# Performance work log

Hardware: AMD Instinct MI355X
Metric: run time of the kernel (lower is better)

Reference implementation:

```python
import jax, jax.numpy as jnp
import numpy as np

# ---- configuration (matches init_kwargs / input_specs) ----
N = 48        # velocity grid points per axis (unum = vnum = wnum)
B = 8         # spatial cells (batch)
QUAD = 8      # radial Gauss-Legendre quadrature points
OMEGA = 0.81  # VHS exponent used in the radial kernel weight r**omega
M_ANG = 5     # sphere-quadrature resolution -> M*(M-1) angle pairs
VMAX = 5.0    # velocity domain [-VMAX, VMAX]^3


def _besselj1(x):
    # Numerical Recipes rational approximation of J1(x), numpy, setup-time only.
    x = np.asarray(x, dtype=np.float64)
    ax = np.abs(x)
    y = x * x
    p1 = x * (72362614232.0 + y * (-7895059235.0 + y * (242396853.1
         + y * (-2972611.439 + y * (15704.48260 + y * (-30.16036606))))))
    q1 = 144725228442.0 + y * (2300535178.0 + y * (18583304.74
         + y * (99447.43394 + y * (376.9991397 + y))))
    small = p1 / q1
    axs = np.where(ax > 0, ax, 1.0)
    z = 8.0 / axs
    y2 = z * z
    p2 = 1.0 + y2 * (0.183105e-2 + y2 * (-0.3516396496e-4
         + y2 * (0.2457520174e-5 + y2 * (-0.240337019e-6))))
    q2 = 0.04687499995 + y2 * (-0.2002690873e-3 + y2 * (0.8449199096e-5
         + y2 * (-0.88228987e-6 + y2 * 0.105787412e-6)))
    xx = axs - 2.356194491  # ax - 3*pi/4
    big = np.sqrt(0.636619772 / axs) * (np.cos(xx) * p2 - z * np.sin(xx) * q2) * np.sign(x)
    return np.where(ax < 8.0, small, big)


def _init_kernel_mode_vector(n, quad_num, omega, m, vmax):
    # Fast spectral method precompute (Mouhot-Pareschi), mirrors init_kernel_mode_vector.
    pi = np.pi
    du = 2.0 * vmax / (n - 1)
    fre = np.arange(-(n // 2), n // 2).astype(np.float64) * (2.0 * pi / (n * du))
    supp = np.sqrt(2.0) * 2.0 * vmax / (3.0 + np.sqrt(2.0))
    xg, wg = np.polynomial.legendre.leggauss(quad_num)  # on [-1,1]
    r = 0.5 * supp * (xg + 1.0)   # radial abscissa on [0, supp]
    gw = 0.5 * supp * wg          # radial weights
    ta = pi / m * np.arange(1, m)      # (m-1,) polar angles
    tb = pi / m * np.arange(1, m + 1)  # (m,)  azimuthal angles
    st = np.sin(ta)[:, None, None, None, None]
    ct = np.cos(ta)[:, None, None, None, None]
    cb = np.cos(tb)[None, :, None, None, None]
    sb = np.sin(tb)[None, :, None, None, None]
    fx = fre[:, None, None]
    fy = fre[None, :, None]
    fz = fre[None, None, :]
    # s[a,b,i,j,k] = <freq, sigma(theta_a, theta2_b)>
    s = st * cb * fx + st * sb * fy + (ct * np.ones_like(sb)) * fz
    phi = np.zeros_like(s)
    for q in range(quad_num):  # small fixed quadrature loop (setup only)
        phi += 2.0 * gw[q] * (r[q] ** omega) * np.cos(s * r[q])
    phi *= st
    s2 = (fx ** 2 + fy ** 2 + fz ** 2) - s ** 2
    pos = s2 > 1e-12
    sr = np.sqrt(np.where(pos, s2, 1.0))
    psi = np.where(pos, 2.0 * pi * supp * _besselj1(supp * sr) / sr, pi * supp ** 2)
    phipsi = (phi * psi).sum(axis=(0, 1))
    t = (m - 1) * m
    return (phi.reshape(t, n, n, n).astype(np.float32),
            psi.reshape(t, n, n, n).astype(np.float32),
            phipsi.astype(np.float32))


def setup_inputs() -> dict:
    key = jax.random.key(0)
    k1, _ = jax.random.split(key)
    phi, psi, phipsi = _init_kernel_mode_vector(N, QUAD, OMEGA, M_ANG, VMAX)
    f = jax.random.uniform(k1, (B, N * N * N), dtype=jnp.float32)
    return {
        "f": f,
        "kn_bzm": jnp.ones((), dtype=jnp.float32),
        "phi": jnp.asarray(phi),
        "psi": jnp.asarray(psi),
        "phipsi": jnp.asarray(phipsi),
        "M": M_ANG,
    }


def reference(f, kn_bzm, phi, psi, phipsi, M):
    # do_collision: reshape flat velocity dim to 3D grid, run collision_fft.
    n = phi.shape[-1]
    axes = (-3, -2, -1)
    f3 = f.reshape(f.shape[:-1] + (n, n, n))
    nvel = n * n * n
    # normalized, shifted spectrum of f
    f_spec = jnp.fft.fftshift(
        jnp.fft.fftn(f3.astype(jnp.complex64), axes=axes) / nvel, axes=axes)
    # gain term: sum over M*(M-1) angle pairs of fft(f_spec*phi_t) * fft(f_spec*psi_t)
    fs = f_spec[..., None, :, :, :]                       # [B, 1, n, n, n]
    fg = (jnp.fft.fftn(fs * phi, axes=axes) *
          jnp.fft.fftn(fs * psi, axes=axes)).sum(axis=-4)  # [B, n, n, n]
    # loss term
    fl = (jnp.fft.fftn(f_spec * phipsi, axes=axes) *
          jnp.fft.fftn(f_spec, axes=axes))
    scale = (4.0 * jnp.pi ** 2) / kn_bzm / (M * M)
    Q = scale * (fg - fl).real
    return Q.reshape(f.shape).astype(f.dtype)
```

## Files before the change

kernel.cpp:

```cpp
#include <hip/hip_runtime.h>
#include <math.h>

#define NN 48
#define NP 49
#define N2 2304
#define N3 110592
#define NB 8
#define NT 20
#define NH 25
#define NSL 7

typedef float2 cplx;

#define CMAC(AR, AI, D, Wv)                                        \
    AR = fmaf((D).x, (Wv).x, AR); AR = fmaf(-(D).y, (Wv).y, AR);   \
    AI = fmaf((D).x, (Wv).y, AI); AI = fmaf((D).y, (Wv).x, AI);

#define CMAC4(AC, D, Wv)                                             \
    (AC).x = fmaf((D).x, (Wv).x, (AC).x); (AC).x = fmaf(-(D).y, (Wv).y, (AC).x); \
    (AC).y = fmaf((D).x, (Wv).y, (AC).y); (AC).y = fmaf((D).y, (Wv).x, (AC).y); \
    (AC).z = fmaf((D).z, (Wv).x, (AC).z); (AC).z = fmaf(-(D).w, (Wv).y, (AC).z); \
    (AC).w = fmaf((D).z, (Wv).y, (AC).w); (AC).w = fmaf((D).w, (Wv).x, (AC).w);

__device__ __forceinline__ void twinit(cplx* W, int t) {
    if (t < NN) {
        float ang = -6.28318530717958647692f * (float)t / (float)NN;
        float s, c;
        sincosf(ang, &s, &c);
        W[t] = make_float2(c, s);
    }
}

__device__ __forceinline__ void radix3_combine(
    float s0r, float s0i, float s1r, float s1i, float s2r, float s2i,
    cplx w1, cplx w2, cplx& X0, cplx& X1, cplx& X2)
{
    float y1r = s1r*w1.x - s1i*w1.y, y1i = s1r*w1.y + s1i*w1.x;
    float y2r = s2r*w2.x - s2i*w2.y, y2i = s2r*w2.y + s2i*w2.x;
    float ar = y1r + y2r, ai = y1i + y2i;
    float br = y1r - y2r, bi = y1i - y2i;
    X0 = make_float2(s0r + ar, s0i + ai);
    float mr = s0r - 0.5f*ar, mi = s0i - 0.5f*ai;
    const float h = 0.86602540378443864676f;
    X1 = make_float2(mr + h*bi, mi - h*br);
    X2 = make_float2(mr - h*bi, mi + h*br);
}

__device__ __forceinline__ void radix3_combine4(
    float4 s0, float4 s1, float4 s2, cplx w1, cplx w2,
    float4& X0, float4& X1, float4& X2)
{
    cplx a0, a1, a2, b0, b1, b2;
    radix3_combine(s0.x, s0.y, s1.x, s1.y, s2.x, s2.y, w1, w2, a0, a1, a2);
    radix3_combine(s0.z, s0.w, s1.z, s1.w, s2.z, s2.w, w1, w2, b0, b1, b2);
    X0 = make_float4(a0.x, a0.y, b0.x, b0.y);
    X1 = make_float4(a1.x, a1.y, b1.x, b1.y);
    X2 = make_float4(a2.x, a2.y, b2.x, b2.y);
}

__device__ __forceinline__ void dft_rows(cplx (*S)[NP], const cplx* W, int t, int shift) {
    const int rg = t >> 4;
    const int j  = t & 15;
    float ar[3][3], ai[3][3];
#pragma unroll
    for (int q = 0; q < 3; ++q)
#pragma unroll
        for (int r = 0; r < 3; ++r) { ar[q][r] = 0.f; ai[q][r] = 0.f; }
    const int step = 3 * j;
    int tw = 0;
#pragma unroll 4
    for (int n1 = 0; n1 < 16; ++n1) {
        cplx w = W[tw];
#pragma unroll
        for (int q = 0; q < 3; ++q) {
            const cplx* row = S[3*rg + q];
            cplx d0 = row[3*n1+0], d1 = row[3*n1+1], d2 = row[3*n1+2];
            CMAC(ar[q][0], ai[q][0], d0, w);
            CMAC(ar[q][1], ai[q][1], d1, w);
            CMAC(ar[q][2], ai[q][2], d2, w);
        }
        tw += step; if (tw >= NN) tw -= NN;
    }
    cplx w1 = W[j], w2 = W[2*j];
    __syncthreads();
    int k0 = j, k1 = j + 16, k2 = j + 32;
    if (shift) { k0 = (k0+24)%NN; k1 = (k1+24)%NN; k2 = (k2+24)%NN; }
#pragma unroll
    for (int q = 0; q < 3; ++q) {
        cplx X0, X1, X2;
        radix3_combine(ar[q][0],ai[q][0],ar[q][1],ai[q][1],ar[q][2],ai[q][2],w1,w2,X0,X1,X2);
        S[3*rg+q][k0] = X0; S[3*rg+q][k1] = X1; S[3*rg+q][k2] = X2;
    }
    __syncthreads();
}

__device__ __forceinline__ void dft_cols(cplx (*S)[NP], const cplx* W, int t, int shift) {
    const int zg = t & 15;
    const int j  = t >> 4;
    float ar[3][3], ai[3][3];
#pragma unroll
    for (int zi = 0; zi < 3; ++zi)
#pragma unroll
        for (int r = 0; r < 3; ++r) { ar[zi][r] = 0.f; ai[zi][r] = 0.f; }
    const int step = 3 * j;
    int tw = 0;
#pragma unroll 4
    for (int n1 = 0; n1 < 16; ++n1) {
        cplx w = W[tw];
#pragma unroll
        for (int r = 0; r < 3; ++r) {
            const cplx* row = S[3*n1 + r];
            cplx d0 = row[3*zg+0], d1 = row[3*zg+1], d2 = row[3*zg+2];
            CMAC(ar[0][r], ai[0][r], d0, w);
            CMAC(ar[1][r], ai[1][r], d1, w);
            CMAC(ar[2][r], ai[2][r], d2, w);
        }
        tw += step; if (tw >= NN) tw -= NN;
    }
    cplx w1 = W[j], w2 = W[2*j];
    __syncthreads();
    int k0 = j, k1 = j + 16, k2 = j + 32;
    if (shift) { k0 = (k0+24)%NN; k1 = (k1+24)%NN; k2 = (k2+24)%NN; }
#pragma unroll
    for (int zi = 0; zi < 3; ++zi) {
        cplx X0, X1, X2;
        radix3_combine(ar[zi][0],ai[zi][0],ar[zi][1],ai[zi][1],ar[zi][2],ai[zi][2],w1,w2,X0,X1,X2);
        S[k0][3*zg+zi] = X0; S[k1][3*zg+zi] = X1; S[k2][3*zg+zi] = X2;
    }
    __syncthreads();
}

__device__ __forceinline__ void dft_rows4(float4 (*S)[NP], const cplx* W, int t) {
    const int rg = t >> 4;
    const int j  = t & 15;
    float4 acc[3][3];
#pragma unroll
    for (int q = 0; q < 3; ++q)
#pragma unroll
        for (int r = 0; r < 3; ++r) acc[q][r] = make_float4(0.f,0.f,0.f,0.f);
    const int step = 3 * j;
    int tw = 0;
    const float4* r0 = S[3*rg + 0];
    const float4* r1 = S[3*rg + 1];
    const float4* r2 = S[3*rg + 2];
#pragma unroll 4
    for (int n1 = 0; n1 < 16; ++n1) {
        cplx w = W[tw];
        float4 d00 = r0[3*n1+0], d01 = r0[3*n1+1], d02 = r0[3*n1+2];
        float4 d10 = r1[3*n1+0], d11 = r1[3*n1+1], d12 = r1[3*n1+2];
        float4 d20 = r2[3*n1+0], d21 = r2[3*n1+1], d22 = r2[3*n1+2];
        CMAC4(acc[0][0], d00, w); CMAC4(acc[0][1], d01, w); CMAC4(acc[0][2], d02, w);
        CMAC4(acc[1][0], d10, w); CMAC4(acc[1][1], d11, w); CMAC4(acc[1][2], d12, w);
        CMAC4(acc[2][0], d20, w); CMAC4(acc[2][1], d21, w); CMAC4(acc[2][2], d22, w);
        tw += step; if (tw >= NN) tw -= NN;
    }
    cplx w1 = W[j], w2 = W[2*j];
    __syncthreads();
#pragma unroll
    for (int q = 0; q < 3; ++q) {
        float4 X0, X1, X2;
        radix3_combine4(acc[q][0], acc[q][1], acc[q][2], w1, w2, X0, X1, X2);
        S[3*rg+q][j] = X0; S[3*rg+q][j+16] = X1; S[3*rg+q][j+32] = X2;
    }
    __syncthreads();
}

__device__ __forceinline__ void dft_cols4(float4 (*S)[NP], const cplx* W, int t) {
    const int zg = t & 15;
    const int j  = t >> 4;
    float4 acc[3][3];
#pragma unroll
    for (int zi = 0; zi < 3; ++zi)
#pragma unroll
        for (int r = 0; r < 3; ++r) acc[zi][r] = make_float4(0.f,0.f,0.f,0.f);
    const int step = 3 * j;
    int tw = 0;
#pragma unroll 4
    for (int n1 = 0; n1 < 16; ++n1) {
        cplx w = W[tw];
#pragma unroll
        for (int r = 0; r < 3; ++r) {
            const float4* row = S[3*n1 + r];
            float4 d0 = row[3*zg+0], d1 = row[3*zg+1], d2 = row[3*zg+2];
            CMAC4(acc[0][r], d0, w);
            CMAC4(acc[1][r], d1, w);
            CMAC4(acc[2][r], d2, w);
        }
        tw += step; if (tw >= NN) tw -= NN;
    }
    cplx w1 = W[j], w2 = W[2*j];
    __syncthreads();
#pragma unroll
    for (int zi = 0; zi < 3; ++zi) {
        float4 X0, X1, X2;
        radix3_combine4(acc[zi][0], acc[zi][1], acc[zi][2], w1, w2, X0, X1, X2);
        S[j][3*zg+zi] = X0; S[j+16][3*zg+zi] = X1; S[j+32][3*zg+zi] = X2;
    }
    __syncthreads();
}

__global__ __launch_bounds__(256)
void kA_f(const float* __restrict__ f, cplx* __restrict__ out) {
    __shared__ cplx S[NN][NP];
    __shared__ cplx W[NN];
    const int x = blockIdx.x, b = blockIdx.y, t = threadIdx.x;
    const float* src = f + (size_t)b * N3 + (size_t)x * N2;
    for (int i = t; i < N2; i += 256) S[i / NN][i % NN] = make_float2(src[i], 0.f);
    twinit(W, t);
    __syncthreads();
    dft_rows(S, W, t, 1);
    dft_cols(S, W, t, 1);
    cplx* dst = out + (size_t)b * N3 + (size_t)x * N2;
    for (int i = t; i < N2; i += 256) dst[i] = S[i / NN][i % NN];
}

__global__ __launch_bounds__(256)
void kB_f(cplx* __restrict__ vol) {
    __shared__ cplx S[NN][NP];
    __shared__ cplx W[NN];
    const int y = blockIdx.x, b = blockIdx.y, t = threadIdx.x;
    cplx* base = vol + (size_t)b * N3 + (size_t)y * NN;
    for (int i = t; i < N2; i += 256) { int xr = i / NN, z = i % NN; S[xr][z] = base[(size_t)xr * N2 + z]; }
    twinit(W, t);
    __syncthreads();
    dft_cols(S, W, t, 1);
    const float inv = 1.f / (float)N3;
    for (int i = t; i < N2; i += 256) {
        int xr = i / NN, z = i % NN;
        cplx v = S[xr][z];
        base[(size_t)xr * N2 + z] = make_float2(v.x * inv, v.y * inv);
    }
}

__global__ __launch_bounds__(256)
void kAB(const cplx* __restrict__ spec,
         const float* __restrict__ phi, const float* __restrict__ psi,
         const float* __restrict__ phipsi,
         float4* __restrict__ vab, int t0) {
    __shared__ float4 S[NN][NP];
    __shared__ cplx W[NN];
    const int ix = blockIdx.x, b = blockIdx.y, lt = blockIdx.z, t = threadIdx.x;
    const int ti = t0 + lt;
    const cplx* src = spec + (size_t)b * N3 + (size_t)ix * N2;
    const float* mp;
    const float* mq;
    if (ti < NT) { mp = phi + (size_t)ti * N3 + (size_t)ix * N2; mq = psi + (size_t)ti * N3 + (size_t)ix * N2; }
    else         { mp = phipsi + (size_t)ix * N2;               mq = (const float*)nullptr; }
    for (int i = t; i < N2; i += 256) {
        cplx v = src[i];
        float p = mp[i];
        float q = mq ? mq[i] : 1.f;
        S[i / NN][i % NN] = make_float4(v.x * p, v.y * p, v.x * q, v.y * q);
    }
    twinit(W, t);
    __syncthreads();
    dft_rows4(S, W, t);
    dft_cols4(S, W, t);
    float4* out = vab + ((size_t)(lt * NB + b) * NH + ix) * N2;
    for (int i = t; i < N2; i += 256) out[i] = S[i / NN][i % NN];
}

__global__ __launch_bounds__(256)
void kB_all(const float4* __restrict__ vab,
            float* __restrict__ out, const float* __restrict__ kn,
            const int* __restrict__ Mv, int t0, int cn) {
    __shared__ float4 SAB[NH][NP];
    __shared__ cplx W[NN];
    const int y = blockIdx.x, b = blockIdx.y, s = blockIdx.z, t = threadIdx.x;
    twinit(W, t);
    const int zg = t & 15, jg = t >> 4;
    float qr[3][3];
#pragma unroll
    for (int m = 0; m < 3; ++m)
#pragma unroll
        for (int zi = 0; zi < 3; ++zi) qr[m][zi] = 0.f;

    for (int lt = s; lt < cn; lt += NSL) {
        const int ti = t0 + lt;
        const float4* pa = vab + (size_t)(lt * NB + b) * NH * N2 + (size_t)y * NN;
        for (int i = t; i < NH * NN; i += 256) {
            int n = i / NN, z = i % NN;
            SAB[n][z] = pa[(size_t)n * N2 + z];
        }
        __syncthreads();
        float sa[3][3], sb[3][3];
#pragma unroll
        for (int m = 0; m < 3; ++m)
#pragma unroll
            for (int zi = 0; zi < 3; ++zi) { sa[m][zi] = 0.f; sb[m][zi] = 0.f; }
        int m0 = jg, m1 = jg + 16, m2 = jg + 32;
        const int s0 = jg, s1 = jg + 16, s2 = jg + 32;
        for (int n = 1; n <= 23; ++n) {
            cplx w0 = W[m0], w1 = W[m1], w2 = W[m2];
#pragma unroll
            for (int zi = 0; zi < 3; ++zi) {
                float4 d = SAB[n][3*zg+zi];
                sa[0][zi] = fmaf(d.x, w0.x, sa[0][zi]); sa[0][zi] = fmaf(-d.y, w0.y, sa[0][zi]);
                sa[1][zi] = fmaf(d.x, w1.x, sa[1][zi]); sa[1][zi] = fmaf(-d.y, w1.y, sa[1][zi]);
                sa[2][zi] = fmaf(d.x, w2.x, sa[2][zi]); sa[2][zi] = fmaf(-d.y, w2.y, sa[2][zi]);
                sb[0][zi] = fmaf(d.z, w0.x, sb[0][zi]); sb[0][zi] = fmaf(-d.w, w0.y, sb[0][zi]);
                sb[1][zi] = fmaf(d.z, w1.x, sb[1][zi]); sb[1][zi] = fmaf(-d.w, w1.y, sb[1][zi]);
                sb[2][zi] = fmaf(d.z, w2.x, sb[2][zi]); sb[2][zi] = fmaf(-d.w, w2.y, sb[2][zi]);
            }
            m0 += s0; if (m0 >= NN) m0 -= NN;
            m1 += s1; if (m1 >= NN) m1 -= NN;
            m2 += s2; if (m2 >= NN) m2 -= NN;
        }
        const float sgn = (jg & 1) ? -1.f : 1.f;
        const float wgt = (ti == NT) ? -1.f : 1.f;
#pragma unroll
        for (int zi = 0; zi < 3; ++zi) {
            float4 e0  = SAB[0][3*zg+zi];
            float4 e24 = SAB[24][3*zg+zi];
            float basea = e0.x + sgn * e24.x;
            float baseb = e0.z + sgn * e24.z;
#pragma unroll
            for (int m = 0; m < 3; ++m) {
                float Ah = basea + 2.f * sa[m][zi];
                float Bh = baseb + 2.f * sb[m][zi];
                qr[m][zi] += wgt * Ah * Bh;
            }
        }
        __syncthreads();
    }
    float mf = (float)(Mv[0] * Mv[0]);
    float scale = 4.f * 3.14159265358979323846f * 3.14159265358979323846f / (kn[0] * mf);
#pragma unroll
    for (int m = 0; m < 3; ++m) {
        int j = jg + 16 * m;
#pragma unroll
        for (int zi = 0; zi < 3; ++zi) {
            int z = 3 * zg + zi;
            size_t idx = (size_t)b * N3 + (size_t)j * N2 + (size_t)y * NN + z;
            atomicAdd(&out[idx], scale * qr[m][zi]);
        }
    }
}

extern "C" void kernel_launch(void* const* d_in, const int* in_sizes, int n_in,
                              void* d_out, int out_size, void* d_ws, size_t ws_size,
                              hipStream_t stream) {
    const float* f      = (const float*)d_in[0];
    const float* kn     = (const float*)d_in[1];
    const float* phi    = (const float*)d_in[2];
    const float* psi    = (const float*)d_in[3];
    const float* phipsi = (const float*)d_in[4];
    const int*   Mv     = (const int*)d_in[5];
    float* out = (float*)d_out;

    char* w = (char*)d_ws;
    const size_t fspecB = (size_t)NB * N3 * sizeof(cplx);
    const size_t perTB  = (size_t)NB * NH * N2 * sizeof(float4);
    cplx* fspec = (cplx*)w;
    char* pool  = w + fspecB;

    const int NTOT = NT + 1;
    size_t avail = (ws_size > fspecB) ? (ws_size - fspecB) : 0;
    int chunk = (int)(avail / perTB);
    if (chunk < 1)    chunk = 1;
    if (chunk > NTOT) chunk = NTOT;
    float4* vab = (float4*)pool;

    hipMemsetAsync(out, 0, (size_t)NB * N3 * sizeof(float), stream);

    kA_f<<<dim3(NN, NB), 256, 0, stream>>>(f, fspec);
    kB_f<<<dim3(NN, NB), 256, 0, stream>>>(fspec);

    for (int t0 = 0; t0 < NTOT; t0 += chunk) {
        int cn = (t0 + chunk <= NTOT) ? chunk : (NTOT - t0);
        kAB<<<dim3(NH, NB, cn), 256, 0, stream>>>(fspec, phi, psi, phipsi, vab, t0);
        kB_all<<<dim3(NN, NB, NSL), 256, 0, stream>>>(vab, out, kn, Mv, t0, cn);
    }
}
```

Before: 290.2 us.

## Process two y-rows per block in kB_all with six output rows per thread

Each kB_all block now handles two y rows: threads split into two halves by y, and each thread computes six j outputs instead of three. Each twiddle load is therefore reused across more FMAs, and the grid is halved. The costs are a larger register footprint (18+36 accumulators), fewer blocks for occupancy, and removal of the NP padding in the shared array, which may raise LDS bank conflicts.

```diff
diff --git a/kernel.cpp b/kernel.cpp
--- a/kernel.cpp
+++ b/kernel.cpp
@@ -264,61 +264,68 @@
 void kB_all(const float4* __restrict__ vab,
             float* __restrict__ out, const float* __restrict__ kn,
             const int* __restrict__ Mv, int t0, int cn) {
-    __shared__ float4 SAB[NH][NP];
+    __shared__ float4 SAB[2][NH][NN];
     __shared__ cplx W[NN];
-    const int y = blockIdx.x, b = blockIdx.y, s = blockIdx.z, t = threadIdx.x;
+    const int yp = blockIdx.x, b = blockIdx.y, s = blockIdx.z, t = threadIdx.x;
     twinit(W, t);
-    const int zg = t & 15, jg = t >> 4;
-    float qr[3][3];
-#pragma unroll
-    for (int m = 0; m < 3; ++m)
-#pragma unroll
-        for (int zi = 0; zi < 3; ++zi) qr[m][zi] = 0.f;
+    const int zg = t & 15;
+    const int jg = (t >> 4) & 7;
+    const int yh = t >> 7;
+    const int y  = 2 * yp + yh;
+    float qr[6][3];
+#pragma unroll
+    for (int k = 0; k < 6; ++k)
+#pragma unroll
+        for (int zi = 0; zi < 3; ++zi) qr[k][zi] = 0.f;
 
     for (int lt = s; lt < cn; lt += NSL) {
         const int ti = t0 + lt;
-        const float4* pa = vab + (size_t)(lt * NB + b) * NH * N2 + (size_t)y * NN;
-        for (int i = t; i < NH * NN; i += 256) {
-            int n = i / NN, z = i % NN;
-            SAB[n][z] = pa[(size_t)n * N2 + z];
+        const float4* base = vab + (size_t)(lt * NB + b) * NH * N2 + (size_t)(2 * yp) * NN;
+        for (int i = t; i < 2 * NH * NN; i += 256) {
+            int yi = i / (NH * NN);
+            int rem = i - yi * (NH * NN);
+            int n = rem / NN, z = rem - n * NN;
+            SAB[yi][n][z] = base[(size_t)n * N2 + yi * NN + z];
         }
         __syncthreads();
-        float sa[3][3], sb[3][3];
-#pragma unroll
-        for (int m = 0; m < 3; ++m)
-#pragma unroll
-            for (int zi = 0; zi < 3; ++zi) { sa[m][zi] = 0.f; sb[m][zi] = 0.f; }
-        int m0 = jg, m1 = jg + 16, m2 = jg + 32;
-        const int s0 = jg, s1 = jg + 16, s2 = jg + 32;
+        float sa[6][3], sb[6][3];
+#pragma unroll
+        for (int k = 0; k < 6; ++k)
+#pragma unroll
+            for (int zi = 0; zi < 3; ++zi) { sa[k][zi] = 0.f; sb[k][zi] = 0.f; }
+        int mm[6];
+#pragma unroll
+        for (int k = 0; k < 6; ++k) mm[k] = jg + 8 * k;
         for (int n = 1; n <= 23; ++n) {
-            cplx w0 = W[m0], w1 = W[m1], w2 = W[m2];
+            cplx w[6];
+#pragma unroll
+            for (int k = 0; k < 6; ++k) {
+                w[k] = W[mm[k]];
+                mm[k] += jg + 8 * k; if (mm[k] >= NN) mm[k] -= NN;
+            }
 #pragma unroll
             for (int zi = 0; zi < 3; ++zi) {
-                float4 d = SAB[n][3*zg+zi];
-                sa[0][zi] = fmaf(d.x, w0.x, sa[0][zi]); sa[0][zi] = fmaf(-d.y, w0.y, sa[0][zi]);
-                sa[1][zi] = fmaf(d.x, w1.x, sa[1][zi]); sa[1][zi] = fmaf(-d.y, w1.y, sa[1][zi]);
-                sa[2][zi] = fmaf(d.x, w2.x, sa[2][zi]); sa[2][zi] = fmaf(-d.y, w2.y, sa[2][zi]);
-                sb[0][zi] = fmaf(d.z, w0.x, sb[0][zi]); sb[0][zi] = fmaf(-d.w, w0.y, sb[0][zi]);
-                sb[1][zi] = fmaf(d.z, w1.x, sb[1][zi]); sb[1][zi] = fmaf(-d.w, w1.y, sb[1][zi]);
-                sb[2][zi] = fmaf(d.z, w2.x, sb[2][zi]); sb[2][zi] = fmaf(-d.w, w2.y, sb[2][zi]);
+                float4 d = SAB[yh][n][3 * zg + zi];
+#pragma unroll
+                for (int k = 0; k < 6; ++k) {
+                    sa[k][zi] = fmaf(d.x, w[k].x, sa[k][zi]); sa[k][zi] = fmaf(-d.y, w[k].y, sa[k][zi]);
+                    sb[k][zi] = fmaf(d.z, w[k].x, sb[k][zi]); sb[k][zi] = fmaf(-d.w, w[k].y, sb[k][zi]);
+                }
             }
-            m0 += s0; if (m0 >= NN) m0 -= NN;
-            m1 += s1; if (m1 >= NN) m1 -= NN;
-            m2 += s2; if (m2 >= NN) m2 -= NN;
         }
         const float sgn = (jg & 1) ? -1.f : 1.f;
         const float wgt = (ti == NT) ? -1.f : 1.f;
 #pragma unroll
         for (int zi = 0; zi < 3; ++zi) {
-            float4 e0  = SAB[0][3*zg+zi];
-            float4 e24 = SAB[24][3*zg+zi];
+            float4 e0  = SAB[yh][0][3 * zg + zi];
+            float4 e24 = SAB[yh][24][3 * zg + zi];
             float basea = e0.x + sgn * e24.x;
             float baseb = e0.z + sgn * e24.z;
 #pragma unroll
-            for (int m = 0; m < 3; ++m) {
-                float Ah = basea + 2.f * sa[m][zi];
-                float Bh = baseb + 2.f * sb[m][zi];
-                qr[m][zi] += wgt * Ah * Bh;
+            for (int k = 0; k < 6; ++k) {
+                float Ah = basea + 2.f * sa[k][zi];
+                float Bh = baseb + 2.f * sb[k][zi];
+                qr[k][zi] += wgt * Ah * Bh;
             }
         }
         __syncthreads();
@@ -326,13 +333,13 @@
     float mf = (float)(Mv[0] * Mv[0]);
     float scale = 4.f * 3.14159265358979323846f * 3.14159265358979323846f / (kn[0] * mf);
 #pragma unroll
-    for (int m = 0; m < 3; ++m) {
-        int j = jg + 16 * m;
+    for (int k = 0; k < 6; ++k) {
+        int j = jg + 8 * k;
 #pragma unroll
         for (int zi = 0; zi < 3; ++zi) {
             int z = 3 * zg + zi;
             size_t idx = (size_t)b * N3 + (size_t)j * N2 + (size_t)y * NN + z;
-            atomicAdd(&out[idx], scale * qr[m][zi]);
+            atomicAdd(&out[idx], scale * qr[k][zi]);
         }
     }
 }
@@ -369,6 +376,6 @@
     for (int t0 = 0; t0 < NTOT; t0 += chunk) {
         int cn = (t0 + chunk <= NTOT) ? chunk : (NTOT - t0);
         kAB<<<dim3(NH, NB, cn), 256, 0, stream>>>(fspec, phi, psi, phipsi, vab, t0);
-        kB_all<<<dim3(NN, NB, NSL), 256, 0, stream>>>(vab, out, kn, Mv, t0, cn);
-    }
-}
+        kB_all<<<dim3(NN / 2, NB, NSL), 256, 0, stream>>>(vab, out, kn, Mv, t0, cn);
+    }
+}
```

New measurement: 312.6 us. 1.08x slower.
